# Kernel tuning notes

Measured on AMD Instinct MI355X. Metric: run time of the kernel, lower is better.

## Reference

```python
import jax, jax.numpy as jnp
import numpy as np

B, L, E, H = 2, 2048, 1024, 16
Dh = E // H  # 64


def setup_inputs() -> dict:
    key = jax.random.key(0)
    ks = jax.random.split(key, 12)
    s = 0.02  # realistic init scale for weights
    inp = {
        "x_q": jax.random.normal(ks[0], (B, L, E), jnp.float32),
        "x_k": jax.random.normal(ks[1], (B, L, E), jnp.float32),
        "x_v": jax.random.normal(ks[2], (B, L, E), jnp.float32),
        # causal mask, broadcast over batch and heads: [1,1,Lq,Lk]
        "mask": jnp.tril(jnp.ones((L, L), jnp.int32))[None, None],
        "Wq": jax.random.normal(ks[3], (E, E), jnp.float32) * s,
        "bq": jnp.zeros((E,), jnp.float32),
        "Wk": jax.random.normal(ks[4], (E, E), jnp.float32) * s,
        "bk": jnp.zeros((E,), jnp.float32),
        "Wv": jax.random.normal(ks[5], (E, E), jnp.float32) * s,
        "bv": jnp.zeros((E,), jnp.float32),
        "Wo": jax.random.normal(ks[6], (E, E), jnp.float32) * s,
        "bo": jnp.zeros((E,), jnp.float32),
    }
    return inp


def reference(x_q, x_k, x_v, mask, Wq, bq, Wk, bk, Wv, bv, Wo, bo):
    N, Lq, _ = x_q.shape
    Lk = x_k.shape[1]
    # Linear projections (torch Linear: x @ W.T + b), split heads -> [B,H,L,Dh]
    q = (x_q @ Wq.T + bq).reshape(N, Lq, H, Dh).transpose(0, 2, 1, 3)
    k = (x_k @ Wk.T + bk).reshape(N, Lk, H, Dh).transpose(0, 2, 1, 3)
    v = (x_v @ Wv.T + bv).reshape(N, Lk, H, Dh).transpose(0, 2, 1, 3)
    # naive SDPA: full [B,H,Lq,Lk] score matrix, exactly as the source module
    scores = jnp.einsum("bhqd,bhkd->bhqk", q, k) / jnp.sqrt(jnp.float32(Dh))
    scores = jnp.where(mask == 0, jnp.float32(-1e9), scores)
    attn = jax.nn.softmax(scores, axis=-1)
    out = jnp.einsum("bhqk,bhkd->bhqd", attn, v)
    out = out.transpose(0, 2, 1, 3).reshape(N, Lq, E)
    return out @ Wo.T + bo
```

## Files before the change

kernel.cpp:

```cpp
#include <hip/hip_runtime.h>
#include <stdint.h>
#include <stddef.h>


#define AS1 __attribute__((address_space(1)))
#define AS3 __attribute__((address_space(3)))

typedef __attribute__((ext_vector_type(8))) __bf16 bf16x8;
typedef __attribute__((ext_vector_type(8))) unsigned short u16x8;
typedef __attribute__((ext_vector_type(4))) unsigned short u16x4;
typedef __attribute__((ext_vector_type(4))) float f32x4;
typedef __attribute__((ext_vector_type(2))) unsigned int u32x2;

#define QSCALE 0.18033688011112042f

static __device__ __forceinline__ unsigned short f2bf(float f) {
  unsigned int u = __builtin_bit_cast(unsigned int, f);
  u += 0x7fffu + ((u >> 16) & 1u);
  return (unsigned short)(u >> 16);
}
static __device__ __forceinline__ unsigned int pkbf(float lo, float hi) {
  return __builtin_amdgcn_perm(__builtin_bit_cast(unsigned int, hi),
                               __builtin_bit_cast(unsigned int, lo), 0x07060302u);
}
static __device__ __forceinline__ void g2l16(const unsigned short* g, unsigned short* l) {
  __builtin_amdgcn_global_load_lds((AS1 void*)g, (AS3 void*)l, 16, 0, 0);
}
static __device__ __forceinline__ float fexp2(float x) {
  return __builtin_amdgcn_exp2f(x);
}

__global__ __launch_bounds__(256) void cvt_kernel(
    const float* __restrict__ s0, const float* __restrict__ s1,
    const float* __restrict__ s2, const float* __restrict__ s3,
    const float* __restrict__ s4, const float* __restrict__ s5,
    const float* __restrict__ s6,
    unsigned short* __restrict__ d0, unsigned short* __restrict__ d1,
    unsigned short* __restrict__ d2, unsigned short* __restrict__ d3,
    unsigned short* __restrict__ d4, unsigned short* __restrict__ d5,
    unsigned short* __restrict__ d6)
{
  const int z = blockIdx.z;
  const float* s; unsigned short* d; int n;
  switch (z) {
    case 0: s = s0; d = d0; n = 4194304; break;
    case 1: s = s1; d = d1; n = 4194304; break;
    case 2: s = s2; d = d2; n = 4194304; break;
    case 3: s = s3; d = d3; n = 1048576; break;
    case 4: s = s4; d = d4; n = 1048576; break;
    case 5: s = s5; d = d5; n = 1048576; break;
    default: s = s6; d = d6; n = 1048576; break;
  }
  int i = (blockIdx.x * 256 + threadIdx.x) * 8;
  if (i >= n) return;
  f32x4 a = *(const f32x4*)(s + i);
  f32x4 b = *(const f32x4*)(s + i + 4);
  u16x8 r;
  r[0] = f2bf(a[0]); r[1] = f2bf(a[1]); r[2] = f2bf(a[2]); r[3] = f2bf(a[3]);
  r[4] = f2bf(b[0]); r[5] = f2bf(b[1]); r[6] = f2bf(b[2]); r[7] = f2bf(b[3]);
  *(u16x8*)(d + i) = r;
}

template<int BM>
static __device__ __forceinline__ void gemm_bt(
    const unsigned short* __restrict__ A,
    const unsigned short* __restrict__ Bw,
    const float* __restrict__ bias,
    unsigned short* __restrict__ outb,
    float* __restrict__ outf,
    int K, int N, int mode, float oscale)
{
  constexpr int MT = BM / 32;
  constexpr int WROWS = BM / 2;
  __shared__ __align__(16) unsigned short As[2][BM * 32];
  __shared__ __align__(16) unsigned short Bs[2][128 * 32];

  const int t    = threadIdx.x;
  const int lane = t & 63;
  const int w    = t >> 6;
  const int quad = lane >> 4;
  const int l15  = lane & 15;
  const int wm   = (w >> 1) * WROWS;
  const int wn   = (w & 1) * 64;
  const int m0   = blockIdx.x * BM;
  const int n0   = blockIdx.y * 128;

  f32x4 acc[MT][4];
  const f32x4 zero = {0.f, 0.f, 0.f, 0.f};
#pragma unroll
  for (int mt = 0; mt < MT; ++mt)
#pragma unroll
    for (int nt = 0; nt < 4; ++nt) acc[mt][nt] = zero;

  auto stage = [&](int buf, int k0) {
#pragma unroll
    for (int i = 0; i < BM / 64; ++i) {
      int c = t + i * 256;
      int row = c >> 2, sl = c & 3;
      int g = sl ^ ((row >> 1) & 3);
      g2l16(A + (size_t)(m0 + row) * K + (k0 + g * 8), &As[buf][c * 8]);
    }
#pragma unroll
    for (int i = 0; i < 2; ++i) {
      int c = t + i * 256;
      int row = c >> 2, sl = c & 3;
      int g = sl ^ ((row >> 1) & 3);
      g2l16(Bw + (size_t)(n0 + row) * K + (k0 + g * 8), &Bs[buf][c * 8]);
    }
  };

  stage(0, 0);
  const int nk = K >> 5;
  for (int kt = 0; kt < nk; ++kt) {
    __syncthreads();
    if (kt + 1 < nk) stage((kt + 1) & 1, (kt + 1) * 32);
    const int b = kt & 1;

    bf16x8 af[MT], bfr[4];
#pragma unroll
    for (int mt = 0; mt < MT; ++mt) {
      int r = wm + mt * 16 + l15;
      af[mt] = *(const bf16x8*)(&As[b][r * 32 + ((quad ^ ((r >> 1) & 3)) * 8)]);
    }
#pragma unroll
    for (int nt = 0; nt < 4; ++nt) {
      int r = wn + nt * 16 + l15;
      bfr[nt] = *(const bf16x8*)(&Bs[b][r * 32 + ((quad ^ ((r >> 1) & 3)) * 8)]);
    }
#pragma unroll
    for (int mt = 0; mt < MT; ++mt)
#pragma unroll
      for (int nt = 0; nt < 4; ++nt)
        acc[mt][nt] = __builtin_amdgcn_mfma_f32_16x16x32_bf16(af[mt], bfr[nt], acc[mt][nt], 0, 0, 0);
  }

#pragma unroll
  for (int nt = 0; nt < 4; ++nt) {
    int n = n0 + wn + nt * 16 + l15;
    float bv = bias[n];
#pragma unroll
    for (int mt = 0; mt < MT; ++mt) {
#pragma unroll
      for (int r = 0; r < 4; ++r) {
        int m = m0 + wm + mt * 16 + quad * 4 + r;
        float val = (acc[mt][nt][r] + bv) * oscale;
        if (mode == 0) {
          outf[(size_t)m * N + n] = val;
        } else {
          int b2 = m >> 11, l = m & 2047, h = n >> 6, d = n & 63;
          size_t idx;
          if (mode == 1) idx = ((size_t)(b2 * 16 + h) * 2048 + l) * 64 + d;
          else           idx = ((size_t)(b2 * 16 + h) * 64 + d) * 2048 + l;
          outb[idx] = f2bf(val);
        }
      }
    }
  }
}

__global__ __launch_bounds__(256, 4) void proj_kernel(
    const unsigned short* __restrict__ xq, const unsigned short* __restrict__ xk,
    const unsigned short* __restrict__ xv,
    const unsigned short* __restrict__ Wq, const float* __restrict__ bq,
    const unsigned short* __restrict__ Wk, const float* __restrict__ bk,
    const unsigned short* __restrict__ Wv, const float* __restrict__ bv,
    unsigned short* __restrict__ Qws, unsigned short* __restrict__ Kws,
    unsigned short* __restrict__ Vtws)
{
  int z = blockIdx.z;
  const unsigned short* A = (z == 0) ? xq : (z == 1) ? xk : xv;
  const unsigned short* W = (z == 0) ? Wq : (z == 1) ? Wk : Wv;
  const float* bias       = (z == 0) ? bq : (z == 1) ? bk : bv;
  unsigned short* out     = (z == 0) ? Qws : (z == 1) ? Kws : Vtws;
  float oscale            = (z == 0) ? QSCALE : 1.0f;
  gemm_bt<128>(A, W, bias, out, nullptr, 1024, 1024, (z == 2) ? 2 : 1, oscale);
}

__global__ __launch_bounds__(256, 4) void oproj_kernel(
    const unsigned short* __restrict__ Ain, const unsigned short* __restrict__ Wo,
    const float* __restrict__ bo, float* __restrict__ out)
{
  gemm_bt<64>(Ain, Wo, bo, nullptr, out, 1024, 1024, 0, 1.0f);
}

__global__ __launch_bounds__(256, 2) void flash_kernel(
    const unsigned short* __restrict__ Q,
    const unsigned short* __restrict__ Km,
    const unsigned short* __restrict__ Vt,
    unsigned short* __restrict__ Ao)
{
  __shared__ __align__(16) unsigned short Ks[2][64 * 64];
  __shared__ __align__(16) unsigned short Vs[2][64 * 64];
  __shared__ __align__(16) unsigned short PsA[4][16 * 64];
  __shared__ __align__(16) unsigned short PsB[4][16 * 64];

  const int t    = threadIdx.x;
  const int lane = t & 63;
  const int w    = t >> 6;
  const int quad = lane >> 4;
  const int l15  = lane & 15;
  const int pi   = blockIdx.x;
  const int bh   = blockIdx.y;
  const int qtA  = 31 - pi;
  const int qtB  = pi;

  const unsigned short* Qb = Q  + (size_t)bh * 2048 * 64;
  const unsigned short* Kb = Km + (size_t)bh * 2048 * 64;
  const unsigned short* Vb = Vt + (size_t)bh * 64 * 2048;
  const int bb = bh >> 4, hh = bh & 15;

  const f32x4 zero = {0.f, 0.f, 0.f, 0.f};

  bf16x8 qfA[2], qfB[2];
#pragma unroll
  for (int s = 0; s < 2; ++s) {
    qfA[s] = *(const bf16x8*)(Qb + (size_t)(qtA * 64 + w * 16 + l15) * 64 + s * 32 + quad * 8);
    qfB[s] = *(const bf16x8*)(Qb + (size_t)(qtB * 64 + w * 16 + l15) * 64 + s * 32 + quad * 8);
  }

  f32x4 oA[4], oB[4];
#pragma unroll
  for (int mt = 0; mt < 4; ++mt) { oA[mt] = zero; oB[mt] = zero; }
  float lA = 0.f, lB = 0.f;

  auto stage = [&](int buf, int kv0) {
#pragma unroll
    for (int i = 0; i < 2; ++i) {
      int c = t + i * 256;
      int row = c >> 3, sl = c & 7;
      int g = sl ^ (row & 7);
      g2l16(Kb + (size_t)(kv0 + row) * 64 + g * 8, &Ks[buf][c * 8]);
      g2l16(Vb + (size_t)row * 2048 + kv0 + g * 8, &Vs[buf][c * 8]);
    }
  };

  stage(0, 0);

  const int pwr = l15 * 64 + (quad & 1) * 4;
  const int pu0 = quad >> 1;
  const int ph  = l15 & 7;

#pragma unroll 1
  for (int it = 0; it <= qtA; ++it) {
    __syncthreads();
    const int cur = it & 1;
    if (it < qtA) stage(cur ^ 1, (it + 1) * 64);
    const bool doB = (it <= qtB);

    bf16x8 kf[4][2];
#pragma unroll
    for (int mt = 0; mt < 4; ++mt) {
      int kv = mt * 16 + l15;
#pragma unroll
      for (int s = 0; s < 2; ++s)
        kf[mt][s] = *(const bf16x8*)(&Ks[cur][kv * 64 + (((s * 4 + quad) ^ (kv & 7)) * 8)]);
    }

    f32x4 sA[4], sB[4];
#pragma unroll
    for (int mt = 0; mt < 4; ++mt) {
      f32x4 z = zero;
      z = __builtin_amdgcn_mfma_f32_16x16x32_bf16(kf[mt][0], qfA[0], z, 0, 0, 0);
      z = __builtin_amdgcn_mfma_f32_16x16x32_bf16(kf[mt][1], qfA[1], z, 0, 0, 0);
      sA[mt] = z;
    }
    if (doB) {
#pragma unroll
      for (int mt = 0; mt < 4; ++mt) {
        f32x4 z = zero;
        z = __builtin_amdgcn_mfma_f32_16x16x32_bf16(kf[mt][0], qfB[0], z, 0, 0, 0);
        z = __builtin_amdgcn_mfma_f32_16x16x32_bf16(kf[mt][1], qfB[1], z, 0, 0, 0);
        sB[mt] = z;
      }
    }

    const int qloc = w * 16 + l15;
    if (it == qtA) {
#pragma unroll
      for (int mt = 0; mt < 4; ++mt)
#pragma unroll
        for (int r = 0; r < 4; ++r)
          if (mt * 16 + quad * 4 + r > qloc) sA[mt][r] = -30000.f;
    }
    if (it == qtB) {
#pragma unroll
      for (int mt = 0; mt < 4; ++mt)
#pragma unroll
        for (int r = 0; r < 4; ++r)
          if (mt * 16 + quad * 4 + r > qloc) sB[mt][r] = -30000.f;
    }

#pragma unroll
    for (int mt = 0; mt < 4; ++mt) {
      float p0 = fexp2(sA[mt][0]), p1 = fexp2(sA[mt][1]);
      float p2 = fexp2(sA[mt][2]), p3 = fexp2(sA[mt][3]);
      lA += (p0 + p1) + (p2 + p3);
      u32x2 pk = {pkbf(p0, p1), pkbf(p2, p3)};
      *(u32x2*)(&PsA[w][pwr + (((mt * 2 + pu0) ^ ph) * 8)]) = pk;
    }
    if (doB) {
#pragma unroll
      for (int mt = 0; mt < 4; ++mt) {
        float p0 = fexp2(sB[mt][0]), p1 = fexp2(sB[mt][1]);
        float p2 = fexp2(sB[mt][2]), p3 = fexp2(sB[mt][3]);
        lB += (p0 + p1) + (p2 + p3);
        u32x2 pk = {pkbf(p0, p1), pkbf(p2, p3)};
        *(u32x2*)(&PsB[w][pwr + (((mt * 2 + pu0) ^ ph) * 8)]) = pk;
      }
    }

    bf16x8 pfA[2], pfB[2];
#pragma unroll
    for (int s = 0; s < 2; ++s)
      pfA[s] = *(const bf16x8*)(&PsA[w][l15 * 64 + (((s * 4 + quad) ^ ph) * 8)]);
    if (doB) {
#pragma unroll
      for (int s = 0; s < 2; ++s)
        pfB[s] = *(const bf16x8*)(&PsB[w][l15 * 64 + (((s * 4 + quad) ^ ph) * 8)]);
    }
#pragma unroll
    for (int mt = 0; mt < 4; ++mt) {
      int dd = mt * 16 + l15;
      bf16x8 vf0 = *(const bf16x8*)(&Vs[cur][dd * 64 + (((quad)     ^ (dd & 7)) * 8)]);
      bf16x8 vf1 = *(const bf16x8*)(&Vs[cur][dd * 64 + (((4 + quad) ^ (dd & 7)) * 8)]);
      oA[mt] = __builtin_amdgcn_mfma_f32_16x16x32_bf16(vf0, pfA[0], oA[mt], 0, 0, 0);
      oA[mt] = __builtin_amdgcn_mfma_f32_16x16x32_bf16(vf1, pfA[1], oA[mt], 0, 0, 0);
      if (doB) {
        oB[mt] = __builtin_amdgcn_mfma_f32_16x16x32_bf16(vf0, pfB[0], oB[mt], 0, 0, 0);
        oB[mt] = __builtin_amdgcn_mfma_f32_16x16x32_bf16(vf1, pfB[1], oB[mt], 0, 0, 0);
      }
    }
  }

#pragma unroll
  for (int half = 0; half < 2; ++half) {
    float lp = half ? lB : lA;
    lp += __shfl_xor(lp, 16, 64);
    lp += __shfl_xor(lp, 32, 64);
    float inv = 1.0f / lp;
    const int qt = half ? qtB : qtA;
    const f32x4* o = half ? oB : oA;
    size_t rowbase = ((size_t)(bb * 2048 + qt * 64 + w * 16 + l15)) * 1024 + hh * 64;
#pragma unroll
    for (int mt = 0; mt < 4; ++mt) {
      u16x4 v;
#pragma unroll
      for (int r = 0; r < 4; ++r) v[r] = f2bf(o[mt][r] * inv);
      *(u16x4*)(Ao + rowbase + mt * 16 + quad * 4) = v;
    }
  }
}

extern "C" void kernel_launch(void* const* d_in, const int* in_sizes, int n_in,
                              void* d_out, int out_size, void* d_ws, size_t ws_size,
                              hipStream_t stream)
{
  (void)in_sizes; (void)n_in; (void)out_size; (void)ws_size;

  const float* xq = (const float*)d_in[0];
  const float* xk = (const float*)d_in[1];
  const float* xv = (const float*)d_in[2];
  const float* Wq = (const float*)d_in[4];
  const float* bq = (const float*)d_in[5];
  const float* Wk = (const float*)d_in[6];
  const float* bk = (const float*)d_in[7];
  const float* Wv = (const float*)d_in[8];
  const float* bv = (const float*)d_in[9];
  const float* Wo = (const float*)d_in[10];
  const float* bo = (const float*)d_in[11];

  const size_t NX = (size_t)4194304;
  const size_t NW = (size_t)1048576;
  unsigned short* Qws  = (unsigned short*)d_ws;
  unsigned short* Kws  = Qws + NX;
  unsigned short* Vtws = Kws + NX;
  unsigned short* xqbf = Vtws + NX;
  unsigned short* xkbf = xqbf + NX;
  unsigned short* xvbf = xkbf + NX;
  unsigned short* Wqbf = xvbf + NX;
  unsigned short* Wkbf = Wqbf + NW;
  unsigned short* Wvbf = Wkbf + NW;
  unsigned short* Wobf = Wvbf + NW;
  unsigned short* Aws  = xqbf;

  dim3 gc(2048, 1, 7);
  cvt_kernel<<<gc, 256, 0, stream>>>(xq, xk, xv, Wq, Wk, Wv, Wo,
                                     xqbf, xkbf, xvbf, Wqbf, Wkbf, Wvbf, Wobf);
  dim3 gp(32, 8, 3);
  proj_kernel<<<gp, 256, 0, stream>>>(xqbf, xkbf, xvbf, Wqbf, bq, Wkbf, bk,
                                      Wvbf, bv, Qws, Kws, Vtws);
  dim3 gf(16, 32, 1);
  flash_kernel<<<gf, 256, 0, stream>>>(Qws, Kws, Vtws, Aws);
  dim3 go(64, 8, 1);
  oproj_kernel<<<go, 256, 0, stream>>>(Aws, Wobf, bo, (float*)d_out);
}
```

Baseline: 225.9 us.

## Fuse fp32 activation conversion into projection GEMM and read K directly

The projection GEMM now streams fp32 activations straight into LDS and packs them to bf16 at fragment-load time. This removes the separate activation conversion pass and its bf16 round trip through memory, so the convert kernel only handles the four weight matrices. The flash kernel drops the K tile from LDS and loads K fragments directly from global memory, and occupancy hints for proj and flash change to 3. In exchange, the projection kernel doubles its A-tile LDS footprint and global read bytes, and K loads become uncoalesced global reads with no LDS reuse.

```diff
diff --git a/kernel.cpp b/kernel.cpp
--- a/kernel.cpp
+++ b/kernel.cpp
@@ -11,6 +11,7 @@
 typedef __attribute__((ext_vector_type(4))) unsigned short u16x4;
 typedef __attribute__((ext_vector_type(4))) float f32x4;
 typedef __attribute__((ext_vector_type(2))) unsigned int u32x2;
+typedef __attribute__((ext_vector_type(4))) unsigned int u32x4;
 
 #define QSCALE 0.18033688011112042f
 
@@ -26,6 +27,9 @@
 static __device__ __forceinline__ void g2l16(const unsigned short* g, unsigned short* l) {
   __builtin_amdgcn_global_load_lds((AS1 void*)g, (AS3 void*)l, 16, 0, 0);
 }
+static __device__ __forceinline__ void g2l16f(const float* g, float* l) {
+  __builtin_amdgcn_global_load_lds((AS1 void*)g, (AS3 void*)l, 16, 0, 0);
+}
 static __device__ __forceinline__ float fexp2(float x) {
   return __builtin_amdgcn_exp2f(x);
 }
@@ -33,26 +37,13 @@
 __global__ __launch_bounds__(256) void cvt_kernel(
     const float* __restrict__ s0, const float* __restrict__ s1,
     const float* __restrict__ s2, const float* __restrict__ s3,
-    const float* __restrict__ s4, const float* __restrict__ s5,
-    const float* __restrict__ s6,
     unsigned short* __restrict__ d0, unsigned short* __restrict__ d1,
-    unsigned short* __restrict__ d2, unsigned short* __restrict__ d3,
-    unsigned short* __restrict__ d4, unsigned short* __restrict__ d5,
-    unsigned short* __restrict__ d6)
+    unsigned short* __restrict__ d2, unsigned short* __restrict__ d3)
 {
   const int z = blockIdx.z;
-  const float* s; unsigned short* d; int n;
-  switch (z) {
-    case 0: s = s0; d = d0; n = 4194304; break;
-    case 1: s = s1; d = d1; n = 4194304; break;
-    case 2: s = s2; d = d2; n = 4194304; break;
-    case 3: s = s3; d = d3; n = 1048576; break;
-    case 4: s = s4; d = d4; n = 1048576; break;
-    case 5: s = s5; d = d5; n = 1048576; break;
-    default: s = s6; d = d6; n = 1048576; break;
-  }
+  const float* s = (z == 0) ? s0 : (z == 1) ? s1 : (z == 2) ? s2 : s3;
+  unsigned short* d = (z == 0) ? d0 : (z == 1) ? d1 : (z == 2) ? d2 : d3;
   int i = (blockIdx.x * 256 + threadIdx.x) * 8;
-  if (i >= n) return;
   f32x4 a = *(const f32x4*)(s + i);
   f32x4 b = *(const f32x4*)(s + i + 4);
   u16x8 r;
@@ -61,9 +52,9 @@
   *(u16x8*)(d + i) = r;
 }
 
-template<int BM>
+template<int BM, bool AF32>
 static __device__ __forceinline__ void gemm_bt(
-    const unsigned short* __restrict__ A,
+    const void* __restrict__ Av,
     const unsigned short* __restrict__ Bw,
     const float* __restrict__ bias,
     unsigned short* __restrict__ outb,
@@ -72,7 +63,8 @@
 {
   constexpr int MT = BM / 32;
   constexpr int WROWS = BM / 2;
-  __shared__ __align__(16) unsigned short As[2][BM * 32];
+  __shared__ __align__(16) float          Asf[AF32 ? 2 : 1][AF32 ? BM * 32 : 1];
+  __shared__ __align__(16) unsigned short Asb[AF32 ? 1 : 2][AF32 ? 1 : BM * 32];
   __shared__ __align__(16) unsigned short Bs[2][128 * 32];
 
   const int t    = threadIdx.x;
@@ -85,6 +77,9 @@
   const int m0   = blockIdx.x * BM;
   const int n0   = blockIdx.y * 128;
 
+  const float* Af          = (const float*)Av;
+  const unsigned short* Ab = (const unsigned short*)Av;
+
   f32x4 acc[MT][4];
   const f32x4 zero = {0.f, 0.f, 0.f, 0.f};
 #pragma unroll
@@ -93,12 +88,22 @@
     for (int nt = 0; nt < 4; ++nt) acc[mt][nt] = zero;
 
   auto stage = [&](int buf, int k0) {
-#pragma unroll
-    for (int i = 0; i < BM / 64; ++i) {
-      int c = t + i * 256;
-      int row = c >> 2, sl = c & 3;
-      int g = sl ^ ((row >> 1) & 3);
-      g2l16(A + (size_t)(m0 + row) * K + (k0 + g * 8), &As[buf][c * 8]);
+    if (AF32) {
+#pragma unroll
+      for (int i = 0; i < BM / 32; ++i) {
+        int c = t + i * 256;
+        int row = c >> 3, sl = c & 7;
+        int g = sl ^ (row & 7);
+        g2l16f(Af + (size_t)(m0 + row) * K + (k0 + g * 4), &Asf[buf][c * 4]);
+      }
+    } else {
+#pragma unroll
+      for (int i = 0; i < BM / 64; ++i) {
+        int c = t + i * 256;
+        int row = c >> 2, sl = c & 3;
+        int g = sl ^ ((row >> 1) & 3);
+        g2l16(Ab + (size_t)(m0 + row) * K + (k0 + g * 8), &Asb[buf][c * 8]);
+      }
     }
 #pragma unroll
     for (int i = 0; i < 2; ++i) {
@@ -120,7 +125,18 @@
 #pragma unroll
     for (int mt = 0; mt < MT; ++mt) {
       int r = wm + mt * 16 + l15;
-      af[mt] = *(const bf16x8*)(&As[b][r * 32 + ((quad ^ ((r >> 1) & 3)) * 8)]);
+      if (AF32) {
+        int h = r & 7;
+        const float* Ar = &Asf[b][r * 32];
+        f32x4 a0 = *(const f32x4*)(Ar + (((2 * quad)     ^ h) * 4));
+        f32x4 a1 = *(const f32x4*)(Ar + (((2 * quad + 1) ^ h) * 4));
+        u32x4 pr;
+        pr[0] = pkbf(a0[0], a0[1]); pr[1] = pkbf(a0[2], a0[3]);
+        pr[2] = pkbf(a1[0], a1[1]); pr[3] = pkbf(a1[2], a1[3]);
+        af[mt] = __builtin_bit_cast(bf16x8, pr);
+      } else {
+        af[mt] = *(const bf16x8*)(&Asb[b][r * 32 + ((quad ^ ((r >> 1) & 3)) * 8)]);
+      }
     }
 #pragma unroll
     for (int nt = 0; nt < 4; ++nt) {
@@ -158,9 +174,9 @@
   }
 }
 
-__global__ __launch_bounds__(256, 4) void proj_kernel(
-    const unsigned short* __restrict__ xq, const unsigned short* __restrict__ xk,
-    const unsigned short* __restrict__ xv,
+__global__ __launch_bounds__(256, 3) void proj_kernel(
+    const float* __restrict__ xq, const float* __restrict__ xk,
+    const float* __restrict__ xv,
     const unsigned short* __restrict__ Wq, const float* __restrict__ bq,
     const unsigned short* __restrict__ Wk, const float* __restrict__ bk,
     const unsigned short* __restrict__ Wv, const float* __restrict__ bv,
@@ -168,28 +184,27 @@
     unsigned short* __restrict__ Vtws)
 {
   int z = blockIdx.z;
-  const unsigned short* A = (z == 0) ? xq : (z == 1) ? xk : xv;
+  const float* A          = (z == 0) ? xq : (z == 1) ? xk : xv;
   const unsigned short* W = (z == 0) ? Wq : (z == 1) ? Wk : Wv;
   const float* bias       = (z == 0) ? bq : (z == 1) ? bk : bv;
   unsigned short* out     = (z == 0) ? Qws : (z == 1) ? Kws : Vtws;
   float oscale            = (z == 0) ? QSCALE : 1.0f;
-  gemm_bt<128>(A, W, bias, out, nullptr, 1024, 1024, (z == 2) ? 2 : 1, oscale);
+  gemm_bt<128, true>(A, W, bias, out, nullptr, 1024, 1024, (z == 2) ? 2 : 1, oscale);
 }
 
 __global__ __launch_bounds__(256, 4) void oproj_kernel(
     const unsigned short* __restrict__ Ain, const unsigned short* __restrict__ Wo,
     const float* __restrict__ bo, float* __restrict__ out)
 {
-  gemm_bt<64>(Ain, Wo, bo, nullptr, out, 1024, 1024, 0, 1.0f);
-}
-
-__global__ __launch_bounds__(256, 2) void flash_kernel(
+  gemm_bt<64, false>(Ain, Wo, bo, nullptr, out, 1024, 1024, 0, 1.0f);
+}
+
+__global__ __launch_bounds__(256, 3) void flash_kernel(
     const unsigned short* __restrict__ Q,
     const unsigned short* __restrict__ Km,
     const unsigned short* __restrict__ Vt,
     unsigned short* __restrict__ Ao)
 {
-  __shared__ __align__(16) unsigned short Ks[2][64 * 64];
   __shared__ __align__(16) unsigned short Vs[2][64 * 64];
   __shared__ __align__(16) unsigned short PsA[4][16 * 64];
   __shared__ __align__(16) unsigned short PsB[4][16 * 64];
@@ -229,7 +244,6 @@
       int c = t + i * 256;
       int row = c >> 3, sl = c & 7;
       int g = sl ^ (row & 7);
-      g2l16(Kb + (size_t)(kv0 + row) * 64 + g * 8, &Ks[buf][c * 8]);
       g2l16(Vb + (size_t)row * 2048 + kv0 + g * 8, &Vs[buf][c * 8]);
     }
   };
@@ -242,18 +256,19 @@
 
 #pragma unroll 1
   for (int it = 0; it <= qtA; ++it) {
+    const int kv0 = it * 64;
     __syncthreads();
     const int cur = it & 1;
-    if (it < qtA) stage(cur ^ 1, (it + 1) * 64);
+    if (it < qtA) stage(cur ^ 1, kv0 + 64);
     const bool doB = (it <= qtB);
 
     bf16x8 kf[4][2];
 #pragma unroll
     for (int mt = 0; mt < 4; ++mt) {
-      int kv = mt * 16 + l15;
+      const unsigned short* Kr = Kb + (size_t)(kv0 + mt * 16 + l15) * 64 + quad * 8;
 #pragma unroll
       for (int s = 0; s < 2; ++s)
-        kf[mt][s] = *(const bf16x8*)(&Ks[cur][kv * 64 + (((s * 4 + quad) ^ (kv & 7)) * 8)]);
+        kf[mt][s] = *(const bf16x8*)(Kr + s * 32);
     }
 
     f32x4 sA[4], sB[4];
@@ -374,20 +389,16 @@
   unsigned short* Qws  = (unsigned short*)d_ws;
   unsigned short* Kws  = Qws + NX;
   unsigned short* Vtws = Kws + NX;
-  unsigned short* xqbf = Vtws + NX;
-  unsigned short* xkbf = xqbf + NX;
-  unsigned short* xvbf = xkbf + NX;
-  unsigned short* Wqbf = xvbf + NX;
+  unsigned short* Aws  = Vtws + NX;
+  unsigned short* Wqbf = Aws + NX;
   unsigned short* Wkbf = Wqbf + NW;
   unsigned short* Wvbf = Wkbf + NW;
   unsigned short* Wobf = Wvbf + NW;
-  unsigned short* Aws  = xqbf;
-
-  dim3 gc(2048, 1, 7);
-  cvt_kernel<<<gc, 256, 0, stream>>>(xq, xk, xv, Wq, Wk, Wv, Wo,
-                                     xqbf, xkbf, xvbf, Wqbf, Wkbf, Wvbf, Wobf);
+
+  dim3 gc(512, 1, 4);
+  cvt_kernel<<<gc, 256, 0, stream>>>(Wq, Wk, Wv, Wo, Wqbf, Wkbf, Wvbf, Wobf);
   dim3 gp(32, 8, 3);
-  proj_kernel<<<gp, 256, 0, stream>>>(xqbf, xkbf, xvbf, Wqbf, bq, Wkbf, bk,
+  proj_kernel<<<gp, 256, 0, stream>>>(xq, xk, xv, Wqbf, bq, Wkbf, bk,
                                       Wvbf, bv, Qws, Kws, Vtws);
   dim3 gf(16, 32, 1);
   flash_kernel<<<gf, 256, 0, stream>>>(Qws, Kws, Vtws, Aws);
```

Measured after the change: 269.1 us. 1.19x slower.
